# Kernel optimization log

Hardware: AMD Instinct MI355X
Metric: run time of the kernel (lower is better)

The kernel has to match this reference:

```python
import jax, jax.numpy as jnp
import numpy as np

N_NODES = 100000
N_EDGES = 1600000
IN_DIM = 128
OUT_DIM = 64


def setup_inputs() -> dict:
    key = jax.random.key(0)
    k1, k2, k3, k4, k5 = jax.random.split(key, 5)
    x = jax.random.normal(k1, (N_NODES, IN_DIM), dtype=jnp.float32)
    src = jax.random.randint(k2, (N_EDGES,), 0, N_NODES)
    dst = jax.random.randint(k3, (N_EDGES,), 0, N_NODES)
    edge_index = jnp.stack([src, dst]).astype(jnp.int64)
    # Glorot-ish init scale for the two GCN weight matrices (bias=False)
    W1 = jax.random.normal(k4, (IN_DIM, OUT_DIM), dtype=jnp.float32) / np.sqrt(IN_DIM)
    W2 = jax.random.normal(k5, (OUT_DIM, OUT_DIM), dtype=jnp.float32) / np.sqrt(OUT_DIM)
    return {"x": x, "edge_index": edge_index, "W1": W1, "W2": W2}


def _gcn_conv(h, W, src, dst, dinv_sqrt, n_nodes):
    """PyG GCNConv (bias=False): out[i] = sum_{j->i} d_j^-1/2 d_i^-1/2 (h_j @ W),
    with self-loops already folded into (src, dst, dinv_sqrt)."""
    h = h @ W                                    # [N, out]
    norm = dinv_sqrt[src] * dinv_sqrt[dst]       # [E+N]
    msg = h[src] * norm[:, None]                 # gather + scale, [E+N, out]
    return jax.ops.segment_sum(msg, dst, num_segments=n_nodes)


def reference(x, edge_index, W1, W2):
    n = x.shape[0]
    # add self-loops (static shape: E + N edges)
    loop = jnp.arange(n, dtype=edge_index.dtype)
    src = jnp.concatenate([edge_index[0], loop])
    dst = jnp.concatenate([edge_index[1], loop])
    # symmetric normalization degrees (in-degree over dst, unit edge weights)
    deg = jax.ops.segment_sum(jnp.ones_like(dst, dtype=x.dtype), dst, num_segments=n)
    dinv_sqrt = jax.lax.rsqrt(deg)  # deg >= 1 because of self-loops
    # dropout is identity in eval mode (training=False)
    h = _gcn_conv(x, W1, src, dst, dinv_sqrt, n)
    h = jax.nn.relu(h)
    out = _gcn_conv(h, W2, src, dst, dinv_sqrt, n)
    return out
```

## Files before the change

kernel.cpp:

```cpp
#include <hip/hip_runtime.h>
#include <hip/hip_bf16.h>

#define IN_DIM  128
#define OUT_DIM 64
#define EPB 4096
#define NBK_MAX 512

typedef short  bf16x8 __attribute__((ext_vector_type(8)));
typedef float  f32x4  __attribute__((ext_vector_type(4)));

__device__ __forceinline__ unsigned short f2bf(float f) {
    unsigned u = __float_as_uint(f);
    u += 0x7fffu + ((u >> 16) & 1u);
    return (unsigned short)(u >> 16);
}
__device__ __forceinline__ float bf2f(unsigned short h) {
    return __uint_as_float((unsigned)h << 16);
}


__global__ __launch_bounds__(256) void k_cnt(const int* __restrict__ dst,
                                             unsigned* __restrict__ colcnt,
                                             int nE, int nbk, int nblk) {
    __shared__ unsigned h[NBK_MAX];
    for (int b = threadIdx.x; b < NBK_MAX; b += 256) h[b] = 0u;
    __syncthreads();
    int blk = blockIdx.x;
    int e0 = blk * EPB, e1 = min(e0 + EPB, nE);
    for (int e = e0 + threadIdx.x; e < e1; e += 256)
        atomicAdd(&h[dst[e] >> 8], 1u);
    __syncthreads();
    for (int b = threadIdx.x; b < nbk; b += 256)
        colcnt[(size_t)b * nblk + blk] = h[b];
}

__global__ __launch_bounds__(512) void k_bsum(unsigned* __restrict__ colcnt,
                                              unsigned* __restrict__ btot,
                                              int nbk, int nblk) {
    __shared__ unsigned s[512];
    int b = blockIdx.x;
    unsigned v = (threadIdx.x < (unsigned)nblk) ? colcnt[(size_t)b * nblk + threadIdx.x] : 0u;
    s[threadIdx.x] = v;
    __syncthreads();
    for (int d = 1; d < 512; d <<= 1) {
        unsigned t = (threadIdx.x >= (unsigned)d) ? s[threadIdx.x - d] : 0u;
        __syncthreads();
        s[threadIdx.x] += t;
        __syncthreads();
    }
    if (threadIdx.x < (unsigned)nblk)
        colcnt[(size_t)b * nblk + threadIdx.x] = s[threadIdx.x] - v;
    if (threadIdx.x == 511) btot[b] = s[511];
}

__global__ __launch_bounds__(512) void k_btots(const unsigned* __restrict__ btot,
                                               unsigned* __restrict__ bbase,
                                               int nbk, int nE) {
    __shared__ unsigned s[512];
    unsigned v = (threadIdx.x < (unsigned)nbk) ? btot[threadIdx.x] : 0u;
    s[threadIdx.x] = v;
    __syncthreads();
    for (int d = 1; d < 512; d <<= 1) {
        unsigned t = (threadIdx.x >= (unsigned)d) ? s[threadIdx.x - d] : 0u;
        __syncthreads();
        s[threadIdx.x] += t;
        __syncthreads();
    }
    if (threadIdx.x < (unsigned)nbk) bbase[threadIdx.x] = s[threadIdx.x] - v;
    if (threadIdx.x == 0) bbase[nbk] = (unsigned)nE;
}

__global__ __launch_bounds__(256) void k_part(const int* __restrict__ src,
                                              const int* __restrict__ dst,
                                              const unsigned* __restrict__ colcnt,
                                              const unsigned* __restrict__ bbase,
                                              unsigned* __restrict__ ebuf,
                                              int nE, int nbk, int nblk) {
    __shared__ unsigned curs[NBK_MAX];
    int blk = blockIdx.x;
    for (int b = threadIdx.x; b < nbk; b += 256)
        curs[b] = bbase[b] + colcnt[(size_t)b * nblk + blk];
    __syncthreads();
    int e0 = blk * EPB, e1 = min(e0 + EPB, nE);
    for (int e = e0 + threadIdx.x; e < e1; e += 256) {
        int d = dst[e], s = src[e];
        unsigned p = atomicAdd(&curs[d >> 8], 1u);
        ebuf[p] = ((unsigned)(d & 255) << 17) | (unsigned)s;
    }
}

__global__ __launch_bounds__(256) void k_fine(const unsigned* __restrict__ ebuf,
                                              const unsigned* __restrict__ bbase,
                                              unsigned* __restrict__ offs,
                                              float* __restrict__ dinv,
                                              int* __restrict__ perm, int n) {
    __shared__ unsigned deg[256], pos[256], cur[256];
    int b = blockIdx.x;
    int node0 = b << 8;
    unsigned ebeg = bbase[b], eend = bbase[b + 1];
    deg[threadIdx.x] = 0u;
    __syncthreads();
    for (unsigned e = ebeg + threadIdx.x; e < eend; e += 256)
        atomicAdd(&deg[ebuf[e] >> 17], 1u);
    __syncthreads();
    unsigned v = deg[threadIdx.x];
    pos[threadIdx.x] = v;
    __syncthreads();
    for (int d = 1; d < 256; d <<= 1) {
        unsigned t = (threadIdx.x >= (unsigned)d) ? pos[threadIdx.x - d] : 0u;
        __syncthreads();
        pos[threadIdx.x] += t;
        __syncthreads();
    }
    unsigned excl = pos[threadIdx.x] - v;
    cur[threadIdx.x] = excl;
    int node = node0 + threadIdx.x;
    if (node < n) {
        offs[node] = ebeg + excl;
        dinv[node] = rsqrtf((float)v + 1.0f);
    }
    __syncthreads();
    for (unsigned e = ebeg + threadIdx.x; e < eend; e += 256) {
        unsigned rec = ebuf[e];
        unsigned p = atomicAdd(&cur[rec >> 17], 1u);
        perm[ebeg + p] = (int)(rec & 0x1FFFFu);
    }
}

template <int KD, bool RELU>
__global__ __launch_bounds__(256) void k_linm(const float* __restrict__ in,
                                              const float* __restrict__ W,
                                              const float* __restrict__ dinv,
                                              unsigned short* __restrict__ outp, int n) {
    constexpr int LDK = KD + 8;
    __shared__ unsigned short WH[64 * LDK];
    __shared__ unsigned short WL[64 * LDK];
    for (int i = threadIdx.x; i < KD * 64; i += 256) {
        int k = i >> 6, c = i & 63;
        float wv = W[i];
        unsigned short h = f2bf(wv);
        WH[c * LDK + k] = h;
        WL[c * LDK + k] = f2bf(wv - bf2f(h));
    }
    __syncthreads();

    int wid = threadIdx.x >> 6, lane = threadIdx.x & 63;
    int r0 = blockIdx.x * 64 + wid * 16;

    constexpr int NK = KD / 32;
    int arow = r0 + (lane & 15);
    int ar = arow < n ? arow : (n - 1);
    int k8 = (lane >> 4) * 8;

    bf16x8 ah[NK], al[NK];
    {
        const float* rp = in + (size_t)ar * KD;
        float dvin = RELU ? dinv[ar] : 0.f;
#pragma unroll
        for (int ks = 0; ks < NK; ++ks) {
            float4 v0 = *(const float4*)(rp + ks * 32 + k8);
            float4 v1 = *(const float4*)(rp + ks * 32 + k8 + 4);
            float xv[8] = {v0.x, v0.y, v0.z, v0.w, v1.x, v1.y, v1.z, v1.w};
#pragma unroll
            for (int j = 0; j < 8; ++j) {
                float f = xv[j];
                if (RELU) f = fmaxf(dvin * f, 0.f);
                unsigned short h = f2bf(f);
                ah[ks][j] = (short)h;
                al[ks][j] = (short)f2bf(f - bf2f(h));
            }
        }
    }

    f32x4 acc[4];
#pragma unroll
    for (int nt = 0; nt < 4; ++nt) {
        int col = nt * 16 + (lane & 15);
        const unsigned short* bh = &WH[col * LDK + k8];
        const unsigned short* bl = &WL[col * LDK + k8];
        f32x4 a = {0.f, 0.f, 0.f, 0.f};
#pragma unroll
        for (int ks = 0; ks < NK; ++ks) {
            bf16x8 Bh = *(const bf16x8*)(bh + ks * 32);
            bf16x8 Bl = *(const bf16x8*)(bl + ks * 32);
            a = __builtin_amdgcn_mfma_f32_16x16x32_bf16(ah[ks], Bh, a, 0, 0, 0);
            a = __builtin_amdgcn_mfma_f32_16x16x32_bf16(ah[ks], Bl, a, 0, 0, 0);
            a = __builtin_amdgcn_mfma_f32_16x16x32_bf16(al[ks], Bh, a, 0, 0, 0);
        }
        acc[nt] = a;
    }

    int orow0 = r0 + (lane >> 4) * 4;
#pragma unroll
    for (int j = 0; j < 4; ++j) {
        int row = orow0 + j;
        if (row < n) {
            float dv = dinv[row];
#pragma unroll
            for (int nt = 0; nt < 4; ++nt)
                outp[(size_t)row * 64 + nt * 16 + (lane & 15)] = f2bf(dv * acc[nt][j]);
        }
    }
}

template <bool FIN>
__global__ __launch_bounds__(256) void k_gather(const unsigned short* __restrict__ hs,
                                                const unsigned* __restrict__ offs,
                                                const int* __restrict__ perm,
                                                const float* __restrict__ dinv,
                                                float* __restrict__ outb,
                                                int n, int nE) {
    int lane = threadIdx.x & 63;
    int g = lane >> 4, li = lane & 15;
    int r = (blockIdx.x * 4 + (threadIdx.x >> 6)) * 4 + g;
    bool nvalid = r < n;
    int rc = nvalid ? r : (n - 1);
    unsigned beg = offs[rc];
    unsigned end = (rc + 1 < n) ? offs[rc + 1] : (unsigned)nE;
    unsigned deg = nvalid ? (end - beg) : 0u;

    float4 q0, q1 = {0.f,0.f,0.f,0.f}, q2 = q1, q3 = q1;
    {
        ushort4 sv = *(const ushort4*)(hs + (size_t)rc * 64 + li * 4);
        q0.x = bf2f(sv.x); q0.y = bf2f(sv.y); q0.z = bf2f(sv.z); q0.w = bf2f(sv.w);
    }

    unsigned m1 = max(deg, (unsigned)__shfl_xor((int)deg, 16));
    unsigned mdeg = max(m1, (unsigned)__shfl_xor((int)m1, 32));

    for (unsigned c0 = 0; c0 < mdeg; c0 += 16) {
        int sl = 0;
        if (c0 + li < deg) sl = perm[beg + c0 + li];
        unsigned rem = mdeg - c0;
        unsigned kmax = rem < 16u ? rem : 16u;
        for (unsigned k = 0; k < kmax; k += 4) {
            int s0 = __shfl(sl, (int)(g * 16) + (int)k);
            int s1 = __shfl(sl, (int)(g * 16) + (int)k + 1);
            int s2 = __shfl(sl, (int)(g * 16) + (int)k + 2);
            int s3 = __shfl(sl, (int)(g * 16) + (int)k + 3);
            unsigned d0 = c0 + k;
            if (d0 < deg) {
                ushort4 v = *(const ushort4*)(hs + (size_t)s0 * 64 + li * 4);
                q0.x += bf2f(v.x); q0.y += bf2f(v.y); q0.z += bf2f(v.z); q0.w += bf2f(v.w);
            }
            if (d0 + 1 < deg) {
                ushort4 v = *(const ushort4*)(hs + (size_t)s1 * 64 + li * 4);
                q1.x += bf2f(v.x); q1.y += bf2f(v.y); q1.z += bf2f(v.z); q1.w += bf2f(v.w);
            }
            if (d0 + 2 < deg) {
                ushort4 v = *(const ushort4*)(hs + (size_t)s2 * 64 + li * 4);
                q2.x += bf2f(v.x); q2.y += bf2f(v.y); q2.z += bf2f(v.z); q2.w += bf2f(v.w);
            }
            if (d0 + 3 < deg) {
                ushort4 v = *(const ushort4*)(hs + (size_t)s3 * 64 + li * 4);
                q3.x += bf2f(v.x); q3.y += bf2f(v.y); q3.z += bf2f(v.z); q3.w += bf2f(v.w);
            }
        }
    }

    if (nvalid) {
        float4 acc;
        acc.x = (q0.x + q1.x) + (q2.x + q3.x);
        acc.y = (q0.y + q1.y) + (q2.y + q3.y);
        acc.z = (q0.z + q1.z) + (q2.z + q3.z);
        acc.w = (q0.w + q1.w) + (q2.w + q3.w);
        if (FIN) {
            float dv = dinv[r];
            acc.x *= dv; acc.y *= dv; acc.z *= dv; acc.w *= dv;
        }
        *(float4*)(outb + (size_t)r * 64 + li * 4) = acc;
    }
}

extern "C" void kernel_launch(void* const* d_in, const int* in_sizes, int n_in,
                              void* d_out, int out_size, void* d_ws, size_t ws_size,
                              hipStream_t stream) {
    const float* x  = (const float*)d_in[0];
    const int*   ei = (const int*)d_in[1];
    const float* W1 = (const float*)d_in[2];
    const float* W2 = (const float*)d_in[3];
    float* out = (float*)d_out;

    int n  = in_sizes[0] / IN_DIM;
    int nE = in_sizes[1] / 2;
    const int* src = ei;
    const int* dst = ei + nE;

    int nbk  = (n + 255) >> 8;
    int nblk = (nE + EPB - 1) / EPB;

    char* w = (char*)d_ws;
    size_t nAl = ((size_t)n * 4 + 255) & ~(size_t)255;
    float*          dinv   = (float*)w;     w += nAl;
    unsigned*       offs   = (unsigned*)w;  w += nAl;
    unsigned*       colcnt = (unsigned*)w;  w += ((size_t)nbk * nblk * 4 + 255) & ~(size_t)255;
    unsigned*       btot   = (unsigned*)w;  w += ((size_t)nbk * 4 + 255) & ~(size_t)255;
    unsigned*       bbase  = (unsigned*)w;  w += ((size_t)(nbk + 1) * 4 + 255) & ~(size_t)255;
    unsigned*       ebuf   = (unsigned*)w;  w += ((size_t)nE * 4 + 255) & ~(size_t)255;
    int*            perm   = (int*)w;       w += ((size_t)nE * 4 + 255) & ~(size_t)255;
    unsigned short* hs     = (unsigned short*)w; w += (size_t)n * 64 * 2;
    float*          agg    = out;

    int gRow = (n + 15) / 16;
    int gMf  = (n + 63) / 64;

    k_cnt  <<<nblk, 256, 0, stream>>>(dst, colcnt, nE, nbk, nblk);
    k_bsum <<<nbk,  512, 0, stream>>>(colcnt, btot, nbk, nblk);
    k_btots<<<1,    512, 0, stream>>>(btot, bbase, nbk, nE);
    k_part <<<nblk, 256, 0, stream>>>(src, dst, colcnt, bbase, ebuf, nE, nbk, nblk);
    k_fine <<<nbk,  256, 0, stream>>>(ebuf, bbase, offs, dinv, perm, n);

    k_linm<IN_DIM, false><<<gMf, 256, 0, stream>>>(x, W1, dinv, hs, n);
    k_gather<false><<<gRow, 256, 0, stream>>>(hs, offs, perm, dinv, agg, n, nE);

    k_linm<OUT_DIM, true><<<gMf, 256, 0, stream>>>(agg, W2, dinv, hs, n);
    k_gather<true><<<gRow, 256, 0, stream>>>(hs, offs, perm, dinv, out, n, nE);
}
```

Measured before the change: 168.4 us.

## Process two rows per 16-lane group in gather with prefetched neighbor indices

The gather kernel now has each 16-lane group aggregate two destination rows instead of one, which halves the grid. It also prefetches the next chunk of neighbor indices from perm before the current chunk is processed, and fully unrolls the 16-step inner loop. The aim is more independent memory loads in flight per wave, to hide gather latency and the dependent perm-load latency. In exchange it raises register pressure and increases divergence, because the loop now runs to the maximum degree across eight rows.

```diff
diff --git a/kernel.cpp b/kernel.cpp
--- a/kernel.cpp
+++ b/kernel.cpp
@@ -212,63 +212,82 @@
                                                 int n, int nE) {
     int lane = threadIdx.x & 63;
     int g = lane >> 4, li = lane & 15;
-    int r = (blockIdx.x * 4 + (threadIdx.x >> 6)) * 4 + g;
-    bool nvalid = r < n;
-    int rc = nvalid ? r : (n - 1);
-    unsigned beg = offs[rc];
-    unsigned end = (rc + 1 < n) ? offs[rc + 1] : (unsigned)nE;
-    unsigned deg = nvalid ? (end - beg) : 0u;
-
-    float4 q0, q1 = {0.f,0.f,0.f,0.f}, q2 = q1, q3 = q1;
+    int base = (blockIdx.x * 4 + (threadIdx.x >> 6)) * 8;
+    int rA = base + g;
+    int rB = base + 4 + g;
+    bool vA = rA < n, vB = rB < n;
+    int rcA = vA ? rA : (n - 1);
+    int rcB = vB ? rB : (n - 1);
+    unsigned begA = offs[rcA];
+    unsigned endA = (rcA + 1 < n) ? offs[rcA + 1] : (unsigned)nE;
+    unsigned begB = offs[rcB];
+    unsigned endB = (rcB + 1 < n) ? offs[rcB + 1] : (unsigned)nE;
+    unsigned degA = vA ? (endA - begA) : 0u;
+    unsigned degB = vB ? (endB - begB) : 0u;
+
+    float4 qA0, qA1 = {0.f,0.f,0.f,0.f}, qA2 = qA1, qA3 = qA1;
+    float4 qB0, qB1 = qA1, qB2 = qA1, qB3 = qA1;
     {
-        ushort4 sv = *(const ushort4*)(hs + (size_t)rc * 64 + li * 4);
-        q0.x = bf2f(sv.x); q0.y = bf2f(sv.y); q0.z = bf2f(sv.z); q0.w = bf2f(sv.w);
-    }
-
-    unsigned m1 = max(deg, (unsigned)__shfl_xor((int)deg, 16));
-    unsigned mdeg = max(m1, (unsigned)__shfl_xor((int)m1, 32));
-
-    for (unsigned c0 = 0; c0 < mdeg; c0 += 16) {
-        int sl = 0;
-        if (c0 + li < deg) sl = perm[beg + c0 + li];
-        unsigned rem = mdeg - c0;
-        unsigned kmax = rem < 16u ? rem : 16u;
-        for (unsigned k = 0; k < kmax; k += 4) {
-            int s0 = __shfl(sl, (int)(g * 16) + (int)k);
-            int s1 = __shfl(sl, (int)(g * 16) + (int)k + 1);
-            int s2 = __shfl(sl, (int)(g * 16) + (int)k + 2);
-            int s3 = __shfl(sl, (int)(g * 16) + (int)k + 3);
-            unsigned d0 = c0 + k;
-            if (d0 < deg) {
-                ushort4 v = *(const ushort4*)(hs + (size_t)s0 * 64 + li * 4);
-                q0.x += bf2f(v.x); q0.y += bf2f(v.y); q0.z += bf2f(v.z); q0.w += bf2f(v.w);
+        ushort4 sv = *(const ushort4*)(hs + (size_t)rcA * 64 + li * 4);
+        qA0.x = bf2f(sv.x); qA0.y = bf2f(sv.y); qA0.z = bf2f(sv.z); qA0.w = bf2f(sv.w);
+        ushort4 tv = *(const ushort4*)(hs + (size_t)rcB * 64 + li * 4);
+        qB0.x = bf2f(tv.x); qB0.y = bf2f(tv.y); qB0.z = bf2f(tv.z); qB0.w = bf2f(tv.w);
+    }
+
+    unsigned dm = max(degA, degB);
+    dm = max(dm, (unsigned)__shfl_xor((int)dm, 16));
+    dm = max(dm, (unsigned)__shfl_xor((int)dm, 32));
+
+    int slA = (li < (int)degA) ? perm[begA + li] : 0;
+    int slB = (li < (int)degB) ? perm[begB + li] : 0;
+
+    for (unsigned c0 = 0; c0 < dm; c0 += 16) {
+        int sAc = slA, sBc = slB;
+        unsigned c1 = c0 + 16;
+        if (c1 < dm) {
+            slA = (c1 + li < degA) ? perm[begA + c1 + li] : 0;
+            slB = (c1 + li < degB) ? perm[begB + c1 + li] : 0;
+        }
+#pragma unroll
+        for (int k = 0; k < 16; ++k) {
+            int sA = __shfl(sAc, g * 16 + k);
+            int sB = __shfl(sBc, g * 16 + k);
+            if (c0 + k < degA) {
+                ushort4 v = *(const ushort4*)(hs + (size_t)sA * 64 + li * 4);
+                float4* q = (k & 2) ? ((k & 1) ? &qA3 : &qA2) : ((k & 1) ? &qA1 : &qA0);
+                q->x += bf2f(v.x); q->y += bf2f(v.y); q->z += bf2f(v.z); q->w += bf2f(v.w);
             }
-            if (d0 + 1 < deg) {
-                ushort4 v = *(const ushort4*)(hs + (size_t)s1 * 64 + li * 4);
-                q1.x += bf2f(v.x); q1.y += bf2f(v.y); q1.z += bf2f(v.z); q1.w += bf2f(v.w);
+            if (c0 + k < degB) {
+                ushort4 v = *(const ushort4*)(hs + (size_t)sB * 64 + li * 4);
+                float4* q = (k & 2) ? ((k & 1) ? &qB3 : &qB2) : ((k & 1) ? &qB1 : &qB0);
+                q->x += bf2f(v.x); q->y += bf2f(v.y); q->z += bf2f(v.z); q->w += bf2f(v.w);
             }
-            if (d0 + 2 < deg) {
-                ushort4 v = *(const ushort4*)(hs + (size_t)s2 * 64 + li * 4);
-                q2.x += bf2f(v.x); q2.y += bf2f(v.y); q2.z += bf2f(v.z); q2.w += bf2f(v.w);
-            }
-            if (d0 + 3 < deg) {
-                ushort4 v = *(const ushort4*)(hs + (size_t)s3 * 64 + li * 4);
-                q3.x += bf2f(v.x); q3.y += bf2f(v.y); q3.z += bf2f(v.z); q3.w += bf2f(v.w);
-            }
-        }
-    }
-
-    if (nvalid) {
+        }
+    }
+
+    if (vA) {
         float4 acc;
-        acc.x = (q0.x + q1.x) + (q2.x + q3.x);
-        acc.y = (q0.y + q1.y) + (q2.y + q3.y);
-        acc.z = (q0.z + q1.z) + (q2.z + q3.z);
-        acc.w = (q0.w + q1.w) + (q2.w + q3.w);
+        acc.x = (qA0.x + qA1.x) + (qA2.x + qA3.x);
+        acc.y = (qA0.y + qA1.y) + (qA2.y + qA3.y);
+        acc.z = (qA0.z + qA1.z) + (qA2.z + qA3.z);
+        acc.w = (qA0.w + qA1.w) + (qA2.w + qA3.w);
         if (FIN) {
-            float dv = dinv[r];
+            float dv = dinv[rA];
             acc.x *= dv; acc.y *= dv; acc.z *= dv; acc.w *= dv;
         }
-        *(float4*)(outb + (size_t)r * 64 + li * 4) = acc;
+        *(float4*)(outb + (size_t)rA * 64 + li * 4) = acc;
+    }
+    if (vB) {
+        float4 acc;
+        acc.x = (qB0.x + qB1.x) + (qB2.x + qB3.x);
+        acc.y = (qB0.y + qB1.y) + (qB2.y + qB3.y);
+        acc.z = (qB0.z + qB1.z) + (qB2.z + qB3.z);
+        acc.w = (qB0.w + qB1.w) + (qB2.w + qB3.w);
+        if (FIN) {
+            float dv = dinv[rB];
+            acc.x *= dv; acc.y *= dv; acc.z *= dv; acc.w *= dv;
+        }
+        *(float4*)(outb + (size_t)rB * 64 + li * 4) = acc;
     }
 }
 
@@ -301,7 +320,7 @@
     unsigned short* hs     = (unsigned short*)w; w += (size_t)n * 64 * 2;
     float*          agg    = out;
 
-    int gRow = (n + 15) / 16;
+    int gRow = (n + 31) / 32;
     int gMf  = (n + 63) / 64;
 
     k_cnt  <<<nblk, 256, 0, stream>>>(dst, colcnt, nE, nbk, nblk);
```

Measured after the change: 169.1 us. No clear change (+0.5%).
